# Performance work log

Measured on AMD Instinct MI355X. Metric: run time of the kernel, lower is better.

The kernel has to match this reference:

```python
import jax, jax.numpy as jnp
import numpy as np

# Constant from livnium.kernel.constants (assumed scalar; value taken as 1.0).
K_O = 1.0
EPS = 1e-12  # F.normalize default eps

B, D, C = 16384, 1024, 3
F_DIM = D + 10  # features = h_final (D) + 10 scalar features


def setup_inputs() -> dict:
    key = jax.random.key(0)
    ks = jax.random.split(key, 8)
    s1 = 1.0 / np.sqrt(F_DIM)
    return {
        "h_final": jax.random.normal(ks[0], (B, D), jnp.float32),
        "v_p": jax.random.normal(ks[1], (B, D), jnp.float32),
        "v_h": jax.random.normal(ks[2], (B, D), jnp.float32),
        "neutral_dir": jax.random.normal(ks[3], (D,), jnp.float32),
        "neutral_scale": jnp.array(1.0, jnp.float32),
        "w1": jax.random.normal(ks[4], (F_DIM, F_DIM), jnp.float32) * s1,
        "b1": jnp.zeros((F_DIM,), jnp.float32),
        "w2": jax.random.normal(ks[5], (C, F_DIM), jnp.float32) * s1,
        "b2": jnp.zeros((C,), jnp.float32),
    }


def _normalize(x, axis):
    n = jnp.linalg.norm(x, axis=axis, keepdims=True)
    return x / jnp.maximum(n, EPS)


def reference(h_final, v_p, v_h, neutral_dir, neutral_scale, w1, b1, w2, b2):
    v_p_n = _normalize(v_p, -1)                      # [B, D]
    v_h_n = _normalize(v_h, -1)                      # [B, D]
    nd_n = _normalize(neutral_dir, 0)                # [D]

    # alignment(): cosine of the unit vectors == batched dot product.
    align = jnp.sum(v_p_n * v_h_n, axis=-1, keepdims=True)        # [B, 1]
    opp = jnp.sum(-v_p_n * v_h_n, axis=-1, keepdims=True)          # [B, 1]
    align_neutral_p = neutral_scale * jnp.sum(v_p_n * nd_n, axis=-1, keepdims=True)
    align_neutral_h = neutral_scale * jnp.sum(v_h_n * nd_n, axis=-1, keepdims=True)

    energy = K_O * ((1.0 + align) * 0.5)
    expose_neg = (1.0 - align) * 0.5
    dist_p_h = jnp.linalg.norm(v_h - v_p, axis=-1, keepdims=True)
    r_p = jnp.linalg.norm(v_p, axis=-1, keepdims=True)
    r_h = jnp.linalg.norm(v_h, axis=-1, keepdims=True)
    r_final = jnp.linalg.norm(h_final, axis=-1, keepdims=True)

    features = jnp.concatenate(
        [h_final, align, opp, energy, expose_neg, dist_p_h,
         r_p, r_h, r_final, align_neutral_p, align_neutral_h], axis=-1)  # [B, D+10]

    hidden = jax.nn.relu(features @ w1.T + b1)
    logits = hidden @ w2.T + b2                      # [B, C]
    return logits
```

## Files before the change

kernel.cpp:

```cpp
#include <hip/hip_runtime.h>
#include <cstdint>
#include <cstddef>

#define B_ROWS 16384
#define D_DIM  1024
#define F_REAL 1034
#define N_PAD  1152
#define K_PAD  1088
#define NK     (K_PAD / 64)
#define EPSN   1e-12f

typedef __bf16 bf16x8 __attribute__((ext_vector_type(8)));
typedef float  f32x4  __attribute__((ext_vector_type(4)));
typedef unsigned short u16;

__device__ __forceinline__ u16 f2bf(float f) {
    __bf16 b = (__bf16)f;
    return __builtin_bit_cast(u16, b);
}

__global__ __launch_bounds__(256)
void prep_kernel(const float* __restrict__ h, const float* __restrict__ vp,
                 const float* __restrict__ vh, const float* __restrict__ nd,
                 const float* __restrict__ nsp, u16* __restrict__ A)
{
    const int row  = blockIdx.x * 4 + (threadIdx.x >> 6);
    const int lane = threadIdx.x & 63;
    const float4* hp  = (const float4*)(h  + (size_t)row * D_DIM);
    const float4* vpp = (const float4*)(vp + (size_t)row * D_DIM);
    const float4* vhp = (const float4*)(vh + (size_t)row * D_DIM);
    const float4* ndp = (const float4*)nd;
    u16* arow = A + (size_t)row * K_PAD;

    float4 pr[4], qr[4], fr[4], nr[4];
    #pragma unroll
    for (int c = 0; c < 4; ++c) pr[c] = vpp[lane + c * 64];
    #pragma unroll
    for (int c = 0; c < 4; ++c) qr[c] = vhp[lane + c * 64];
    #pragma unroll
    for (int c = 0; c < 4; ++c) fr[c] = hp[lane + c * 64];
    #pragma unroll
    for (int c = 0; c < 4; ++c) nr[c] = ndp[lane + c * 64];

    float s_pp = 0.f, s_hh = 0.f, s_pv = 0.f, s_ff = 0.f;
    float s_dd = 0.f, s_pn = 0.f, s_hn = 0.f, s_nn = 0.f;

    #pragma unroll
    for (int c = 0; c < 4; ++c) {
        float4 p = pr[c], q = qr[c], f = fr[c], n = nr[c];
        s_pp += p.x*p.x + p.y*p.y + p.z*p.z + p.w*p.w;
        s_hh += q.x*q.x + q.y*q.y + q.z*q.z + q.w*q.w;
        s_pv += p.x*q.x + p.y*q.y + p.z*q.z + p.w*q.w;
        s_ff += f.x*f.x + f.y*f.y + f.z*f.z + f.w*f.w;
        float dx = q.x-p.x, dy = q.y-p.y, dz = q.z-p.z, dw = q.w-p.w;
        s_dd += dx*dx + dy*dy + dz*dz + dw*dw;
        s_pn += p.x*n.x + p.y*n.y + p.z*n.z + p.w*n.w;
        s_hn += q.x*n.x + q.y*n.y + q.z*n.z + q.w*n.w;
        s_nn += n.x*n.x + n.y*n.y + n.z*n.z + n.w*n.w;

        ushort4 ho;
        ho.x = f2bf(f.x); ho.y = f2bf(f.y); ho.z = f2bf(f.z); ho.w = f2bf(f.w);
        *(ushort4*)(arow + (lane + c * 64) * 4) = ho;
    }

    #pragma unroll
    for (int m = 32; m >= 1; m >>= 1) {
        s_pp += __shfl_xor(s_pp, m, 64);
        s_hh += __shfl_xor(s_hh, m, 64);
        s_pv += __shfl_xor(s_pv, m, 64);
        s_ff += __shfl_xor(s_ff, m, 64);
        s_dd += __shfl_xor(s_dd, m, 64);
        s_pn += __shfl_xor(s_pn, m, 64);
        s_hn += __shfl_xor(s_hn, m, 64);
        s_nn += __shfl_xor(s_nn, m, 64);
    }

    if (lane == 0) {
        float np_ = sqrtf(s_pp), nh_ = sqrtf(s_hh), nf = sqrtf(s_ff);
        float npc = fmaxf(np_, EPSN), nhc = fmaxf(nh_, EPSN);
        float nnc = fmaxf(sqrtf(s_nn), EPSN);
        float align = s_pv / (npc * nhc);
        float ns = nsp[0];
        u16 fo[64];
        fo[0] = f2bf(align);
        fo[1] = f2bf(-align);
        fo[2] = f2bf(0.5f * (1.0f + align));
        fo[3] = f2bf(0.5f * (1.0f - align));
        fo[4] = f2bf(sqrtf(s_dd));
        fo[5] = f2bf(np_);
        fo[6] = f2bf(nh_);
        fo[7] = f2bf(nf);
        fo[8] = f2bf(ns * s_pn / (npc * nnc));
        fo[9] = f2bf(ns * s_hn / (nhc * nnc));
        #pragma unroll
        for (int i = 10; i < 64; ++i) fo[i] = 0;
        #pragma unroll
        for (int i = 0; i < 8; ++i)
            *(uint4*)(arow + D_DIM + i * 8) = *(uint4*)(fo + i * 8);
    }
}

__global__ __launch_bounds__(256)
void convw_kernel(const float* __restrict__ w1, u16* __restrict__ Bm)
{
    const int i = blockIdx.x;
    for (int j = threadIdx.x; j < K_PAD; j += 256) {
        float v = (i < F_REAL && j < F_REAL) ? w1[(size_t)i * F_REAL + j] : 0.0f;
        Bm[(size_t)i * K_PAD + j] = f2bf(v);
    }
}

__global__ __launch_bounds__(256)
void initout_kernel(const float* __restrict__ b2, float* __restrict__ out)
{
    int i = blockIdx.x * 256 + threadIdx.x;
    if (i < B_ROWS * 3) out[i] = b2[i % 3];
}

__global__ __launch_bounds__(256)
void gemm_kernel(const u16* __restrict__ A,
                 const u16* __restrict__ Bm,
                 const float* __restrict__ b1, const float* __restrict__ w2,
                 float* __restrict__ out)
{
    __shared__ __bf16 As[2 * 64 * 32];
    __shared__ __bf16 Bs[2 * 128 * 32];

    const int tid  = threadIdx.x;
    const int lane = tid & 63;
    const int wave = tid >> 6;
    const int wm = wave >> 1, wn = wave & 1;
    const int bm = blockIdx.x, bn = blockIdx.y;

    const u16* gaA;
    __bf16*    lA;
    {
        int row = tid >> 2;
        int kc  = (tid & 3) ^ (row & 3);
        gaA = A + (size_t)(bm * 64 + row) * K_PAD + kc * 8;
        lA  = As + tid * 8;
    }
    const u16* gaB[2];
    __bf16*    lB[2];
    #pragma unroll
    for (int o = 0; o < 2; ++o) {
        int s   = o * 256 + tid;
        int row = s >> 2;
        int kc  = (s & 3) ^ (row & 3);
        gaB[o] = Bm + (size_t)(bn * 128 + row) * K_PAD + kc * 8;
        lB[o]  = Bs + s * 8;
    }

    const int col  = lane & 15;
    const int quad = lane >> 4;
    const int swz  = quad ^ (col & 3);
    int aoff[2], boff[4];
    #pragma unroll
    for (int i = 0; i < 2; ++i)
        aoff[i] = ((wm * 32 + i * 16 + col) * 4 + swz) * 8;
    #pragma unroll
    for (int j = 0; j < 4; ++j)
        boff[j] = ((wn * 64 + j * 16 + col) * 4 + swz) * 8;

    f32x4 acc[2][4];
    #pragma unroll
    for (int i = 0; i < 2; ++i)
        #pragma unroll
        for (int j = 0; j < 4; ++j)
            acc[i][j] = (f32x4){0.f, 0.f, 0.f, 0.f};

    uint4 a0_0, a1_0, b00_0, b01_0, b10_0, b11_0;
    uint4 a0_1, a1_1, b00_1, b01_1, b10_1, b11_1;

#define LOAD_STAGE(st, ko)                                                    \
    do {                                                                      \
        a0_##st  = *(const uint4*)(gaA + (ko));                               \
        a1_##st  = *(const uint4*)(gaA + (ko) + 32);                          \
        b00_##st = *(const uint4*)(gaB[0] + (ko));                            \
        b01_##st = *(const uint4*)(gaB[0] + (ko) + 32);                       \
        b10_##st = *(const uint4*)(gaB[1] + (ko));                            \
        b11_##st = *(const uint4*)(gaB[1] + (ko) + 32);                       \
    } while (0)

#define WRITE_STAGE(st)                                                       \
    do {                                                                      \
        *(uint4*)(lA)           = a0_##st;                                    \
        *(uint4*)(lA + 2048)    = a1_##st;                                    \
        *(uint4*)(lB[0])        = b00_##st;                                   \
        *(uint4*)(lB[0] + 4096) = b01_##st;                                   \
        *(uint4*)(lB[1])        = b10_##st;                                   \
        *(uint4*)(lB[1] + 4096) = b11_##st;                                   \
    } while (0)

#define COMPUTE_TILE                                                          \
    do {                                                                      \
        _Pragma("unroll")                                                     \
        for (int h = 0; h < 2; ++h) {                                         \
            const __bf16* Ab = As + h * 2048;                                 \
            const __bf16* Bb = Bs + h * 4096;                                 \
            bf16x8 av[2], bv[4];                                              \
            _Pragma("unroll")                                                 \
            for (int i = 0; i < 2; ++i) av[i] = *(const bf16x8*)(Ab + aoff[i]); \
            _Pragma("unroll")                                                 \
            for (int j = 0; j < 4; ++j) bv[j] = *(const bf16x8*)(Bb + boff[j]); \
            _Pragma("unroll")                                                 \
            for (int i = 0; i < 2; ++i)                                       \
                _Pragma("unroll")                                             \
                for (int j = 0; j < 4; ++j)                                   \
                    acc[i][j] = __builtin_amdgcn_mfma_f32_16x16x32_bf16(      \
                                    av[i], bv[j], acc[i][j], 0, 0, 0);        \
        }                                                                     \
    } while (0)

    LOAD_STAGE(0, 0);
    LOAD_STAGE(1, 64);
    WRITE_STAGE(0);
    __syncthreads();

    for (int kt = 0; kt < NK; kt += 2) {
        if (kt + 2 < NK) LOAD_STAGE(0, (kt + 2) * 64);
        COMPUTE_TILE;
        if (kt + 1 < NK) {
            __syncthreads();
            WRITE_STAGE(1);
            __syncthreads();

            if (kt + 3 < NK) LOAD_STAGE(1, (kt + 3) * 64);
            COMPUTE_TILE;
            if (kt + 2 < NK) {
                __syncthreads();
                WRITE_STAGE(0);
                __syncthreads();
            }
        }
    }

    float bias[4], w20[4], w21[4], w22[4];
    #pragma unroll
    for (int ni = 0; ni < 4; ++ni) {
        int n = bn * 128 + wn * 64 + ni * 16 + col;
        bool v = n < F_REAL;
        bias[ni] = v ? b1[n] : 0.0f;
        w20[ni]  = v ? w2[n] : 0.0f;
        w21[ni]  = v ? w2[F_REAL + n] : 0.0f;
        w22[ni]  = v ? w2[2 * F_REAL + n] : 0.0f;
    }
    #pragma unroll
    for (int mi = 0; mi < 2; ++mi) {
        float c0[4] = {0,0,0,0}, c1[4] = {0,0,0,0}, c2[4] = {0,0,0,0};
        #pragma unroll
        for (int ni = 0; ni < 4; ++ni) {
            #pragma unroll
            for (int r = 0; r < 4; ++r) {
                float hd = fmaxf(acc[mi][ni][r] + bias[ni], 0.0f);
                c0[r] += hd * w20[ni];
                c1[r] += hd * w21[ni];
                c2[r] += hd * w22[ni];
            }
        }
        #pragma unroll
        for (int m = 8; m >= 1; m >>= 1) {
            #pragma unroll
            for (int r = 0; r < 4; ++r) {
                c0[r] += __shfl_xor(c0[r], m, 64);
                c1[r] += __shfl_xor(c1[r], m, 64);
                c2[r] += __shfl_xor(c2[r], m, 64);
            }
        }
        if (col == 0) {
            int gm = bm * 64 + wm * 32 + mi * 16 + quad * 4;
            #pragma unroll
            for (int r = 0; r < 4; ++r) {
                atomicAdd(out + (size_t)(gm + r) * 3 + 0, c0[r]);
                atomicAdd(out + (size_t)(gm + r) * 3 + 1, c1[r]);
                atomicAdd(out + (size_t)(gm + r) * 3 + 2, c2[r]);
            }
        }
    }
}

extern "C" void kernel_launch(void* const* d_in, const int* in_sizes, int n_in,
                              void* d_out, int out_size, void* d_ws, size_t ws_size,
                              hipStream_t stream)
{
    const float* h  = (const float*)d_in[0];
    const float* vp = (const float*)d_in[1];
    const float* vh = (const float*)d_in[2];
    const float* nd = (const float*)d_in[3];
    const float* ns = (const float*)d_in[4];
    const float* w1 = (const float*)d_in[5];
    const float* b1 = (const float*)d_in[6];
    const float* w2 = (const float*)d_in[7];
    const float* b2 = (const float*)d_in[8];
    float* out = (float*)d_out;

    u16* Afull = (u16*)d_ws;
    u16* Bfull = Afull + (size_t)B_ROWS * K_PAD;

    prep_kernel<<<B_ROWS / 4, 256, 0, stream>>>(h, vp, vh, nd, ns, Afull);
    convw_kernel<<<N_PAD, 256, 0, stream>>>(w1, Bfull);
    initout_kernel<<<(B_ROWS * 3 + 255) / 256, 256, 0, stream>>>(b2, out);
    gemm_kernel<<<dim3(B_ROWS / 64, N_PAD / 128), 256, 0, stream>>>(
        Afull, Bfull, b1, w2, out);
}
```

Baseline: 291.9 us.

## Enlarge GEMM block tile to 128x128 and split prep rows across two waves

The GEMM block tile grows from 64x128 to 128x128, so each wave now computes a 64x64 sub-tile with 4x4 MFMA accumulators. This doubles A reuse per B load and halves the grid rows, and the LDS swizzle is changed to match the new layout. The prep kernel now splits each row across two waves with an LDS reduction to spread the memory-bound work over more wavefronts. The risks are higher register pressure under launch_bounds(256,2) and fewer GEMM blocks to fill the GPU.

```diff
diff --git a/kernel.cpp b/kernel.cpp
--- a/kernel.cpp
+++ b/kernel.cpp
@@ -24,44 +24,51 @@
                  const float* __restrict__ vh, const float* __restrict__ nd,
                  const float* __restrict__ nsp, u16* __restrict__ A)
 {
-    const int row  = blockIdx.x * 4 + (threadIdx.x >> 6);
-    const int lane = threadIdx.x & 63;
+    __shared__ float red[4][8];
+    const int tid  = threadIdx.x;
+    const int wave = tid >> 6;
+    const int lane = tid & 63;
+    const int row  = blockIdx.x * 2 + (wave >> 1);
+    const int half = wave & 1;
+    const int base = half * 128;
+
     const float4* hp  = (const float4*)(h  + (size_t)row * D_DIM);
     const float4* vpp = (const float4*)(vp + (size_t)row * D_DIM);
     const float4* vhp = (const float4*)(vh + (size_t)row * D_DIM);
     const float4* ndp = (const float4*)nd;
     u16* arow = A + (size_t)row * K_PAD;
 
-    float4 pr[4], qr[4], fr[4], nr[4];
-    #pragma unroll
-    for (int c = 0; c < 4; ++c) pr[c] = vpp[lane + c * 64];
-    #pragma unroll
-    for (int c = 0; c < 4; ++c) qr[c] = vhp[lane + c * 64];
-    #pragma unroll
-    for (int c = 0; c < 4; ++c) fr[c] = hp[lane + c * 64];
-    #pragma unroll
-    for (int c = 0; c < 4; ++c) nr[c] = ndp[lane + c * 64];
-
-    float s_pp = 0.f, s_hh = 0.f, s_pv = 0.f, s_ff = 0.f;
-    float s_dd = 0.f, s_pn = 0.f, s_hn = 0.f, s_nn = 0.f;
-
-    #pragma unroll
-    for (int c = 0; c < 4; ++c) {
-        float4 p = pr[c], q = qr[c], f = fr[c], n = nr[c];
-        s_pp += p.x*p.x + p.y*p.y + p.z*p.z + p.w*p.w;
-        s_hh += q.x*q.x + q.y*q.y + q.z*q.z + q.w*q.w;
-        s_pv += p.x*q.x + p.y*q.y + p.z*q.z + p.w*q.w;
-        s_ff += f.x*f.x + f.y*f.y + f.z*f.z + f.w*f.w;
-        float dx = q.x-p.x, dy = q.y-p.y, dz = q.z-p.z, dw = q.w-p.w;
-        s_dd += dx*dx + dy*dy + dz*dz + dw*dw;
-        s_pn += p.x*n.x + p.y*n.y + p.z*n.z + p.w*n.w;
-        s_hn += q.x*n.x + q.y*n.y + q.z*n.z + q.w*n.w;
-        s_nn += n.x*n.x + n.y*n.y + n.z*n.z + n.w*n.w;
-
-        ushort4 ho;
-        ho.x = f2bf(f.x); ho.y = f2bf(f.y); ho.z = f2bf(f.z); ho.w = f2bf(f.w);
-        *(ushort4*)(arow + (lane + c * 64) * 4) = ho;
-    }
+    float4 p0 = vpp[base + lane], p1 = vpp[base + 64 + lane];
+    float4 q0 = vhp[base + lane], q1 = vhp[base + 64 + lane];
+    float4 f0 = hp [base + lane], f1 = hp [base + 64 + lane];
+    float4 n0 = ndp[base + lane], n1 = ndp[base + 64 + lane];
+    float ns = nsp[0];
+    __builtin_amdgcn_sched_barrier(0);
+
+    float s_pp = p0.x*p0.x + p0.y*p0.y + p0.z*p0.z + p0.w*p0.w
+               + p1.x*p1.x + p1.y*p1.y + p1.z*p1.z + p1.w*p1.w;
+    float s_hh = q0.x*q0.x + q0.y*q0.y + q0.z*q0.z + q0.w*q0.w
+               + q1.x*q1.x + q1.y*q1.y + q1.z*q1.z + q1.w*q1.w;
+    float s_pv = p0.x*q0.x + p0.y*q0.y + p0.z*q0.z + p0.w*q0.w
+               + p1.x*q1.x + p1.y*q1.y + p1.z*q1.z + p1.w*q1.w;
+    float s_ff = f0.x*f0.x + f0.y*f0.y + f0.z*f0.z + f0.w*f0.w
+               + f1.x*f1.x + f1.y*f1.y + f1.z*f1.z + f1.w*f1.w;
+    float dx0 = q0.x-p0.x, dy0 = q0.y-p0.y, dz0 = q0.z-p0.z, dw0 = q0.w-p0.w;
+    float dx1 = q1.x-p1.x, dy1 = q1.y-p1.y, dz1 = q1.z-p1.z, dw1 = q1.w-p1.w;
+    float s_dd = dx0*dx0 + dy0*dy0 + dz0*dz0 + dw0*dw0
+               + dx1*dx1 + dy1*dy1 + dz1*dz1 + dw1*dw1;
+    float s_pn = p0.x*n0.x + p0.y*n0.y + p0.z*n0.z + p0.w*n0.w
+               + p1.x*n1.x + p1.y*n1.y + p1.z*n1.z + p1.w*n1.w;
+    float s_hn = q0.x*n0.x + q0.y*n0.y + q0.z*n0.z + q0.w*n0.w
+               + q1.x*n1.x + q1.y*n1.y + q1.z*n1.z + q1.w*n1.w;
+    float s_nn = n0.x*n0.x + n0.y*n0.y + n0.z*n0.z + n0.w*n0.w
+               + n1.x*n1.x + n1.y*n1.y + n1.z*n1.z + n1.w*n1.w;
+
+    ushort4 h0c, h1c;
+    h0c.x = f2bf(f0.x); h0c.y = f2bf(f0.y); h0c.z = f2bf(f0.z); h0c.w = f2bf(f0.w);
+    h1c.x = f2bf(f1.x); h1c.y = f2bf(f1.y); h1c.z = f2bf(f1.z); h1c.w = f2bf(f1.w);
+    *(ushort4*)(arow + (base + lane) * 4)      = h0c;
+    *(ushort4*)(arow + (base + 64 + lane) * 4) = h1c;
 
     #pragma unroll
     for (int m = 32; m >= 1; m >>= 1) {
@@ -76,22 +83,38 @@
     }
 
     if (lane == 0) {
-        float np_ = sqrtf(s_pp), nh_ = sqrtf(s_hh), nf = sqrtf(s_ff);
+        red[wave][0] = s_pp; red[wave][1] = s_hh; red[wave][2] = s_pv;
+        red[wave][3] = s_ff; red[wave][4] = s_dd; red[wave][5] = s_pn;
+        red[wave][6] = s_hn; red[wave][7] = s_nn;
+    }
+    __syncthreads();
+
+    if (half == 0 && lane == 0) {
+        const int ow = wave + 1;
+        float t_pp = red[wave][0] + red[ow][0];
+        float t_hh = red[wave][1] + red[ow][1];
+        float t_pv = red[wave][2] + red[ow][2];
+        float t_ff = red[wave][3] + red[ow][3];
+        float t_dd = red[wave][4] + red[ow][4];
+        float t_pn = red[wave][5] + red[ow][5];
+        float t_hn = red[wave][6] + red[ow][6];
+        float t_nn = red[wave][7] + red[ow][7];
+
+        float np_ = sqrtf(t_pp), nh_ = sqrtf(t_hh), nf = sqrtf(t_ff);
         float npc = fmaxf(np_, EPSN), nhc = fmaxf(nh_, EPSN);
-        float nnc = fmaxf(sqrtf(s_nn), EPSN);
-        float align = s_pv / (npc * nhc);
-        float ns = nsp[0];
+        float nnc = fmaxf(sqrtf(t_nn), EPSN);
+        float align = t_pv / (npc * nhc);
         u16 fo[64];
         fo[0] = f2bf(align);
         fo[1] = f2bf(-align);
         fo[2] = f2bf(0.5f * (1.0f + align));
         fo[3] = f2bf(0.5f * (1.0f - align));
-        fo[4] = f2bf(sqrtf(s_dd));
+        fo[4] = f2bf(sqrtf(t_dd));
         fo[5] = f2bf(np_);
         fo[6] = f2bf(nh_);
         fo[7] = f2bf(nf);
-        fo[8] = f2bf(ns * s_pn / (npc * nnc));
-        fo[9] = f2bf(ns * s_hn / (nhc * nnc));
+        fo[8] = f2bf(ns * t_pn / (npc * nnc));
+        fo[9] = f2bf(ns * t_hn / (nhc * nnc));
         #pragma unroll
         for (int i = 10; i < 64; ++i) fo[i] = 0;
         #pragma unroll
@@ -117,13 +140,13 @@
     if (i < B_ROWS * 3) out[i] = b2[i % 3];
 }
 
-__global__ __launch_bounds__(256)
+__global__ __launch_bounds__(256, 2)
 void gemm_kernel(const u16* __restrict__ A,
                  const u16* __restrict__ Bm,
                  const float* __restrict__ b1, const float* __restrict__ w2,
                  float* __restrict__ out)
 {
-    __shared__ __bf16 As[2 * 64 * 32];
+    __shared__ __bf16 As[2 * 128 * 32];
     __shared__ __bf16 Bs[2 * 128 * 32];
 
     const int tid  = threadIdx.x;
@@ -132,79 +155,77 @@
     const int wm = wave >> 1, wn = wave & 1;
     const int bm = blockIdx.x, bn = blockIdx.y;
 
-    const u16* gaA;
-    __bf16*    lA;
-    {
-        int row = tid >> 2;
-        int kc  = (tid & 3) ^ (row & 3);
-        gaA = A + (size_t)(bm * 64 + row) * K_PAD + kc * 8;
-        lA  = As + tid * 8;
-    }
+    const int srow = tid >> 2;
+    const int kc   = (tid & 3) ^ ((srow >> 1) & 3);
+    const u16* gaA[2];
     const u16* gaB[2];
-    __bf16*    lB[2];
+    __bf16 *lA[2], *lB[2];
     #pragma unroll
     for (int o = 0; o < 2; ++o) {
-        int s   = o * 256 + tid;
-        int row = s >> 2;
-        int kc  = (s & 3) ^ (row & 3);
-        gaB[o] = Bm + (size_t)(bn * 128 + row) * K_PAD + kc * 8;
-        lB[o]  = Bs + s * 8;
+        gaA[o] = A  + (size_t)(bm * 128 + o * 64 + srow) * K_PAD + kc * 8;
+        gaB[o] = Bm + (size_t)(bn * 128 + o * 64 + srow) * K_PAD + kc * 8;
+        lA[o]  = As + (o * 256 + tid) * 8;
+        lB[o]  = Bs + (o * 256 + tid) * 8;
     }
 
     const int col  = lane & 15;
     const int quad = lane >> 4;
-    const int swz  = quad ^ (col & 3);
-    int aoff[2], boff[4];
-    #pragma unroll
-    for (int i = 0; i < 2; ++i)
-        aoff[i] = ((wm * 32 + i * 16 + col) * 4 + swz) * 8;
+    const int swz  = quad ^ ((col >> 1) & 3);
+    int aoff[4], boff[4];
+    #pragma unroll
+    for (int i = 0; i < 4; ++i)
+        aoff[i] = ((wm * 64 + i * 16 + col) * 4 + swz) * 8;
     #pragma unroll
     for (int j = 0; j < 4; ++j)
         boff[j] = ((wn * 64 + j * 16 + col) * 4 + swz) * 8;
 
-    f32x4 acc[2][4];
-    #pragma unroll
-    for (int i = 0; i < 2; ++i)
+    f32x4 acc[4][4];
+    #pragma unroll
+    for (int i = 0; i < 4; ++i)
         #pragma unroll
         for (int j = 0; j < 4; ++j)
             acc[i][j] = (f32x4){0.f, 0.f, 0.f, 0.f};
 
-    uint4 a0_0, a1_0, b00_0, b01_0, b10_0, b11_0;
-    uint4 a0_1, a1_1, b00_1, b01_1, b10_1, b11_1;
+    uint4 a0_0, a0_1, a0_2, a0_3, b0_0, b0_1, b0_2, b0_3;
+    uint4 a1_0, a1_1, a1_2, a1_3, b1_0, b1_1, b1_2, b1_3;
 
 #define LOAD_STAGE(st, ko)                                                    \
     do {                                                                      \
-        a0_##st  = *(const uint4*)(gaA + (ko));                               \
-        a1_##st  = *(const uint4*)(gaA + (ko) + 32);                          \
-        b00_##st = *(const uint4*)(gaB[0] + (ko));                            \
-        b01_##st = *(const uint4*)(gaB[0] + (ko) + 32);                       \
-        b10_##st = *(const uint4*)(gaB[1] + (ko));                            \
-        b11_##st = *(const uint4*)(gaB[1] + (ko) + 32);                       \
+        a##st##_0 = *(const uint4*)(gaA[0] + (ko));                           \
+        a##st##_1 = *(const uint4*)(gaA[0] + (ko) + 32);                      \
+        a##st##_2 = *(const uint4*)(gaA[1] + (ko));                           \
+        a##st##_3 = *(const uint4*)(gaA[1] + (ko) + 32);                      \
+        b##st##_0 = *(const uint4*)(gaB[0] + (ko));                           \
+        b##st##_1 = *(const uint4*)(gaB[0] + (ko) + 32);                      \
+        b##st##_2 = *(const uint4*)(gaB[1] + (ko));                           \
+        b##st##_3 = *(const uint4*)(gaB[1] + (ko) + 32);                      \
     } while (0)
 
 #define WRITE_STAGE(st)                                                       \
     do {                                                                      \
-        *(uint4*)(lA)           = a0_##st;                                    \
-        *(uint4*)(lA + 2048)    = a1_##st;                                    \
-        *(uint4*)(lB[0])        = b00_##st;                                   \
-        *(uint4*)(lB[0] + 4096) = b01_##st;                                   \
-        *(uint4*)(lB[1])        = b10_##st;                                   \
-        *(uint4*)(lB[1] + 4096) = b11_##st;                                   \
+        *(uint4*)(lA[0])        = a##st##_0;                                  \
+        *(uint4*)(lA[0] + 4096) = a##st##_1;                                  \
+        *(uint4*)(lA[1])        = a##st##_2;                                  \
+        *(uint4*)(lA[1] + 4096) = a##st##_3;                                  \
+        *(uint4*)(lB[0])        = b##st##_0;                                  \
+        *(uint4*)(lB[0] + 4096) = b##st##_1;                                  \
+        *(uint4*)(lB[1])        = b##st##_2;                                  \
+        *(uint4*)(lB[1] + 4096) = b##st##_3;                                  \
     } while (0)
 
 #define COMPUTE_TILE                                                          \
     do {                                                                      \
         _Pragma("unroll")                                                     \
-        for (int h = 0; h < 2; ++h) {                                         \
-            const __bf16* Ab = As + h * 2048;                                 \
-            const __bf16* Bb = Bs + h * 4096;                                 \
-            bf16x8 av[2], bv[4];                                              \
+        for (int hh = 0; hh < 2; ++hh) {                                      \
+            const __bf16* Ab = As + hh * 4096;                                \
+            const __bf16* Bb = Bs + hh * 4096;                                \
+            bf16x8 av[4], bv[4];                                              \
             _Pragma("unroll")                                                 \
-            for (int i = 0; i < 2; ++i) av[i] = *(const bf16x8*)(Ab + aoff[i]); \
+            for (int i = 0; i < 4; ++i) av[i] = *(const bf16x8*)(Ab + aoff[i]); \
             _Pragma("unroll")                                                 \
             for (int j = 0; j < 4; ++j) bv[j] = *(const bf16x8*)(Bb + boff[j]); \
             _Pragma("unroll")                                                 \
-            for (int i = 0; i < 2; ++i)                                       \
+            for (int i = 0; i < 4; ++i)                                       \
                 _Pragma("unroll")                                             \
                 for (int j = 0; j < 4; ++j)                                   \
                     acc[i][j] = __builtin_amdgcn_mfma_f32_16x16x32_bf16(      \
@@ -246,7 +267,7 @@
         w22[ni]  = v ? w2[2 * F_REAL + n] : 0.0f;
     }
     #pragma unroll
-    for (int mi = 0; mi < 2; ++mi) {
+    for (int mi = 0; mi < 4; ++mi) {
         float c0[4] = {0,0,0,0}, c1[4] = {0,0,0,0}, c2[4] = {0,0,0,0};
         #pragma unroll
         for (int ni = 0; ni < 4; ++ni) {
@@ -268,7 +289,7 @@
             }
         }
         if (col == 0) {
-            int gm = bm * 64 + wm * 32 + mi * 16 + quad * 4;
+            int gm = bm * 128 + wm * 64 + mi * 16 + quad * 4;
             #pragma unroll
             for (int r = 0; r < 4; ++r) {
                 atomicAdd(out + (size_t)(gm + r) * 3 + 0, c0[r]);
@@ -297,9 +318,9 @@
     u16* Afull = (u16*)d_ws;
     u16* Bfull = Afull + (size_t)B_ROWS * K_PAD;
 
-    prep_kernel<<<B_ROWS / 4, 256, 0, stream>>>(h, vp, vh, nd, ns, Afull);
+    prep_kernel<<<B_ROWS / 2, 256, 0, stream>>>(h, vp, vh, nd, ns, Afull);
     convw_kernel<<<N_PAD, 256, 0, stream>>>(w1, Bfull);
     initout_kernel<<<(B_ROWS * 3 + 255) / 256, 256, 0, stream>>>(b2, out);
-    gemm_kernel<<<dim3(B_ROWS / 64, N_PAD / 128), 256, 0, stream>>>(
+    gemm_kernel<<<dim3(B_ROWS / 128, N_PAD / 128), 256, 0, stream>>>(
         Afull, Bfull, b1, w2, out);
 }
```

After: 296.6 us. No clear change (+1.6%).

## Process four rows per wave with prefetch, fuse output init, change LDS swizzle

Applied to the files above, without the earlier changes.

The prep kernel now has each wave handle four rows. It double-buffers the register loads of the next row while the current one is being reduced, and loads and reduces neutral_dir once per wave instead of once per row. The separate bias-init kernel is folded into the weight-conversion kernel, which removes one launch. The GEMM's LDS XOR swizzle now uses different index bits, aimed at cutting bank conflicts on the MFMA fragment reads. The double-buffered prefetch raises register use in the prep kernel.

```diff
diff --git a/kernel.cpp b/kernel.cpp
--- a/kernel.cpp
+++ b/kernel.cpp
@@ -24,97 +24,120 @@
                  const float* __restrict__ vh, const float* __restrict__ nd,
                  const float* __restrict__ nsp, u16* __restrict__ A)
 {
-    const int row  = blockIdx.x * 4 + (threadIdx.x >> 6);
-    const int lane = threadIdx.x & 63;
-    const float4* hp  = (const float4*)(h  + (size_t)row * D_DIM);
-    const float4* vpp = (const float4*)(vp + (size_t)row * D_DIM);
-    const float4* vhp = (const float4*)(vh + (size_t)row * D_DIM);
+    const int tid  = threadIdx.x;
+    const int lane = tid & 63;
+    const int wg   = blockIdx.x * 4 + (tid >> 6);
+    const int r0   = wg * 4;
+
     const float4* ndp = (const float4*)nd;
-    u16* arow = A + (size_t)row * K_PAD;
-
-    float4 pr[4], qr[4], fr[4], nr[4];
-    #pragma unroll
-    for (int c = 0; c < 4; ++c) pr[c] = vpp[lane + c * 64];
-    #pragma unroll
-    for (int c = 0; c < 4; ++c) qr[c] = vhp[lane + c * 64];
-    #pragma unroll
-    for (int c = 0; c < 4; ++c) fr[c] = hp[lane + c * 64];
-    #pragma unroll
-    for (int c = 0; c < 4; ++c) nr[c] = ndp[lane + c * 64];
-
-    float s_pp = 0.f, s_hh = 0.f, s_pv = 0.f, s_ff = 0.f;
-    float s_dd = 0.f, s_pn = 0.f, s_hn = 0.f, s_nn = 0.f;
-
-    #pragma unroll
-    for (int c = 0; c < 4; ++c) {
-        float4 p = pr[c], q = qr[c], f = fr[c], n = nr[c];
-        s_pp += p.x*p.x + p.y*p.y + p.z*p.z + p.w*p.w;
-        s_hh += q.x*q.x + q.y*q.y + q.z*q.z + q.w*q.w;
-        s_pv += p.x*q.x + p.y*q.y + p.z*q.z + p.w*q.w;
-        s_ff += f.x*f.x + f.y*f.y + f.z*f.z + f.w*f.w;
-        float dx = q.x-p.x, dy = q.y-p.y, dz = q.z-p.z, dw = q.w-p.w;
-        s_dd += dx*dx + dy*dy + dz*dz + dw*dw;
-        s_pn += p.x*n.x + p.y*n.y + p.z*n.z + p.w*n.w;
-        s_hn += q.x*n.x + q.y*n.y + q.z*n.z + q.w*n.w;
-        s_nn += n.x*n.x + n.y*n.y + n.z*n.z + n.w*n.w;
-
-        ushort4 ho;
-        ho.x = f2bf(f.x); ho.y = f2bf(f.y); ho.z = f2bf(f.z); ho.w = f2bf(f.w);
-        *(ushort4*)(arow + (lane + c * 64) * 4) = ho;
-    }
-
-    #pragma unroll
-    for (int m = 32; m >= 1; m >>= 1) {
-        s_pp += __shfl_xor(s_pp, m, 64);
-        s_hh += __shfl_xor(s_hh, m, 64);
-        s_pv += __shfl_xor(s_pv, m, 64);
-        s_ff += __shfl_xor(s_ff, m, 64);
-        s_dd += __shfl_xor(s_dd, m, 64);
-        s_pn += __shfl_xor(s_pn, m, 64);
-        s_hn += __shfl_xor(s_hn, m, 64);
-        s_nn += __shfl_xor(s_nn, m, 64);
-    }
-
-    if (lane == 0) {
-        float np_ = sqrtf(s_pp), nh_ = sqrtf(s_hh), nf = sqrtf(s_ff);
-        float npc = fmaxf(np_, EPSN), nhc = fmaxf(nh_, EPSN);
-        float nnc = fmaxf(sqrtf(s_nn), EPSN);
-        float align = s_pv / (npc * nhc);
-        float ns = nsp[0];
-        u16 fo[64];
-        fo[0] = f2bf(align);
-        fo[1] = f2bf(-align);
-        fo[2] = f2bf(0.5f * (1.0f + align));
-        fo[3] = f2bf(0.5f * (1.0f - align));
-        fo[4] = f2bf(sqrtf(s_dd));
-        fo[5] = f2bf(np_);
-        fo[6] = f2bf(nh_);
-        fo[7] = f2bf(nf);
-        fo[8] = f2bf(ns * s_pn / (npc * nnc));
-        fo[9] = f2bf(ns * s_hn / (nhc * nnc));
-        #pragma unroll
-        for (int i = 10; i < 64; ++i) fo[i] = 0;
-        #pragma unroll
-        for (int i = 0; i < 8; ++i)
-            *(uint4*)(arow + D_DIM + i * 8) = *(uint4*)(fo + i * 8);
-    }
+    float4 n[4];
+    #pragma unroll
+    for (int c = 0; c < 4; ++c) n[c] = ndp[lane + c * 64];
+    const float ns = nsp[0];
+
+    float s_nn = 0.f;
+    #pragma unroll
+    for (int c = 0; c < 4; ++c)
+        s_nn += n[c].x*n[c].x + n[c].y*n[c].y + n[c].z*n[c].z + n[c].w*n[c].w;
+    #pragma unroll
+    for (int m = 32; m >= 1; m >>= 1) s_nn += __shfl_xor(s_nn, m, 64);
+    const float nnc = fmaxf(sqrtf(s_nn), EPSN);
+
+    float4 P[2][4], Q[2][4], F[2][4];
+
+#define LOADR(st, r)                                                          \
+    do {                                                                      \
+        const float4* vpp = (const float4*)(vp + (size_t)(r) * D_DIM);        \
+        const float4* vhp = (const float4*)(vh + (size_t)(r) * D_DIM);        \
+        const float4* hp  = (const float4*)(h  + (size_t)(r) * D_DIM);        \
+        _Pragma("unroll")                                                     \
+        for (int c = 0; c < 4; ++c) P[st][c] = vpp[lane + c * 64];            \
+        _Pragma("unroll")                                                     \
+        for (int c = 0; c < 4; ++c) Q[st][c] = vhp[lane + c * 64];            \
+        _Pragma("unroll")                                                     \
+        for (int c = 0; c < 4; ++c) F[st][c] = hp[lane + c * 64];             \
+    } while (0)
+
+    LOADR(0, r0);
+    #pragma unroll
+    for (int i = 0; i < 4; ++i) {
+        const int st = i & 1;
+        if (i + 1 < 4) LOADR(((i + 1) & 1), r0 + i + 1);
+        __builtin_amdgcn_sched_barrier(0);
+
+        float s_pp = 0.f, s_hh = 0.f, s_pv = 0.f, s_ff = 0.f;
+        float s_dd = 0.f, s_pn = 0.f, s_hn = 0.f;
+        #pragma unroll
+        for (int c = 0; c < 4; ++c) {
+            float4 p = P[st][c], q = Q[st][c], f = F[st][c], nn = n[c];
+            s_pp += p.x*p.x + p.y*p.y + p.z*p.z + p.w*p.w;
+            s_hh += q.x*q.x + q.y*q.y + q.z*q.z + q.w*q.w;
+            s_pv += p.x*q.x + p.y*q.y + p.z*q.z + p.w*q.w;
+            s_ff += f.x*f.x + f.y*f.y + f.z*f.z + f.w*f.w;
+            float dx = q.x-p.x, dy = q.y-p.y, dz = q.z-p.z, dw = q.w-p.w;
+            s_dd += dx*dx + dy*dy + dz*dz + dw*dw;
+            s_pn += p.x*nn.x + p.y*nn.y + p.z*nn.z + p.w*nn.w;
+            s_hn += q.x*nn.x + q.y*nn.y + q.z*nn.z + q.w*nn.w;
+        }
+
+        u16* arow = A + (size_t)(r0 + i) * K_PAD;
+        #pragma unroll
+        for (int c = 0; c < 4; ++c) {
+            ushort4 hc;
+            hc.x = f2bf(F[st][c].x); hc.y = f2bf(F[st][c].y);
+            hc.z = f2bf(F[st][c].z); hc.w = f2bf(F[st][c].w);
+            *(ushort4*)(arow + (lane + c * 64) * 4) = hc;
+        }
+
+        #pragma unroll
+        for (int m = 32; m >= 1; m >>= 1) {
+            s_pp += __shfl_xor(s_pp, m, 64);
+            s_hh += __shfl_xor(s_hh, m, 64);
+            s_pv += __shfl_xor(s_pv, m, 64);
+            s_ff += __shfl_xor(s_ff, m, 64);
+            s_dd += __shfl_xor(s_dd, m, 64);
+            s_pn += __shfl_xor(s_pn, m, 64);
+            s_hn += __shfl_xor(s_hn, m, 64);
+        }
+
+        if (lane == 0) {
+            float np_ = sqrtf(s_pp), nh_ = sqrtf(s_hh), nf = sqrtf(s_ff);
+            float npc = fmaxf(np_, EPSN), nhc = fmaxf(nh_, EPSN);
+            float align = s_pv / (npc * nhc);
+            u16 fo[64];
+            fo[0] = f2bf(align);
+            fo[1] = f2bf(-align);
+            fo[2] = f2bf(0.5f * (1.0f + align));
+            fo[3] = f2bf(0.5f * (1.0f - align));
+            fo[4] = f2bf(sqrtf(s_dd));
+            fo[5] = f2bf(np_);
+            fo[6] = f2bf(nh_);
+            fo[7] = f2bf(nf);
+            fo[8] = f2bf(ns * s_pn / (npc * nnc));
+            fo[9] = f2bf(ns * s_hn / (nhc * nnc));
+            #pragma unroll
+            for (int k = 10; k < 64; ++k) fo[k] = 0;
+            #pragma unroll
+            for (int k = 0; k < 8; ++k)
+                *(uint4*)(arow + D_DIM + k * 8) = *(uint4*)(fo + k * 8);
+        }
+    }
+#undef LOADR
 }
 
 __global__ __launch_bounds__(256)
-void convw_kernel(const float* __restrict__ w1, u16* __restrict__ Bm)
+void convw_kernel(const float* __restrict__ w1, u16* __restrict__ Bm,
+                  const float* __restrict__ b2, float* __restrict__ out)
 {
     const int i = blockIdx.x;
     for (int j = threadIdx.x; j < K_PAD; j += 256) {
         float v = (i < F_REAL && j < F_REAL) ? w1[(size_t)i * F_REAL + j] : 0.0f;
         Bm[(size_t)i * K_PAD + j] = f2bf(v);
     }
-}
-
-__global__ __launch_bounds__(256)
-void initout_kernel(const float* __restrict__ b2, float* __restrict__ out)
-{
-    int i = blockIdx.x * 256 + threadIdx.x;
-    if (i < B_ROWS * 3) out[i] = b2[i % 3];
+    if (i < 192) {
+        int o = i * 256 + threadIdx.x;
+        out[o] = b2[o % 3];
+    }
 }
 
 __global__ __launch_bounds__(256)
@@ -136,7 +159,7 @@
     __bf16*    lA;
     {
         int row = tid >> 2;
-        int kc  = (tid & 3) ^ (row & 3);
+        int kc  = (tid & 3) ^ ((tid >> 3) & 3);
         gaA = A + (size_t)(bm * 64 + row) * K_PAD + kc * 8;
         lA  = As + tid * 8;
     }
@@ -146,14 +169,14 @@
     for (int o = 0; o < 2; ++o) {
         int s   = o * 256 + tid;
         int row = s >> 2;
-        int kc  = (s & 3) ^ (row & 3);
+        int kc  = (s & 3) ^ ((s >> 3) & 3);
         gaB[o] = Bm + (size_t)(bn * 128 + row) * K_PAD + kc * 8;
         lB[o]  = Bs + s * 8;
     }
 
     const int col  = lane & 15;
     const int quad = lane >> 4;
-    const int swz  = quad ^ (col & 3);
+    const int swz  = quad ^ ((col >> 1) & 3);
     int aoff[2], boff[4];
     #pragma unroll
     for (int i = 0; i < 2; ++i)
@@ -277,6 +300,9 @@
             }
         }
     }
+#undef LOAD_STAGE
+#undef WRITE_STAGE
+#undef COMPUTE_TILE
 }
 
 extern "C" void kernel_launch(void* const* d_in, const int* in_sizes, int n_in,
@@ -297,9 +323,8 @@
     u16* Afull = (u16*)d_ws;
     u16* Bfull = Afull + (size_t)B_ROWS * K_PAD;
 
-    prep_kernel<<<B_ROWS / 4, 256, 0, stream>>>(h, vp, vh, nd, ns, Afull);
-    convw_kernel<<<N_PAD, 256, 0, stream>>>(w1, Bfull);
-    initout_kernel<<<(B_ROWS * 3 + 255) / 256, 256, 0, stream>>>(b2, out);
+    prep_kernel<<<1024, 256, 0, stream>>>(h, vp, vh, nd, ns, Afull);
+    convw_kernel<<<N_PAD, 256, 0, stream>>>(w1, Bfull, b2, out);
     gemm_kernel<<<dim3(B_ROWS / 64, N_PAD / 128), 256, 0, stream>>>(
         Afull, Bfull, b1, w2, out);
 }
```

After: 290.0 us. No clear change (-0.7%).
